# Optimization experiments

Hardware: AMD Instinct MI355X
Metric: run time of the kernel (lower is better)

The kernel has to match this reference:

```python
import jax, jax.numpy as jnp
import numpy as np

N = 1000000          # total nodes (events)
F = 64               # node feature dim
E = 4000000          # total edges
NB = 16              # number of graphs in batch
GRID = 64            # voxels per spatial dim; voxel_size = 1/GRID over [0,1)^2
VOXEL_SIZE = 1.0 / GRID
S = NB * GRID * GRID # fixed cluster-id space (batch-major voxel ids)


def setup_inputs() -> dict:
    key = jax.random.key(0)
    k1, k2, k3, k4 = jax.random.split(key, 4)
    x = jax.random.normal(k1, (N, F), dtype=jnp.float32)
    pos = jax.random.uniform(k2, (N, 2), dtype=jnp.float32)
    batch = jnp.sort(jax.random.randint(k3, (N,), 0, NB, dtype=jnp.int32))
    edge_index = jax.random.randint(k4, (2, E), 0, N, dtype=jnp.int32)
    return {"x": x, "pos": pos, "batch": batch, "edge_index": edge_index}


def reference(x, pos, batch, edge_index):
    # ---- voxel_grid: hash each node into a (batch, vy, vx) voxel cluster ----
    start = pos.min(axis=0)                                   # PyG uses global min as grid origin
    vox = jnp.clip(jnp.floor((pos - start) / VOXEL_SIZE).astype(jnp.int32), 0, GRID - 1)
    cluster = batch * (GRID * GRID) + vox[:, 1] * GRID + vox[:, 0]   # [N]

    # ---- max_pool: scatter-max features, scatter-mean positions ----
    x_pool = jax.ops.segment_max(x, cluster, num_segments=S)         # [S, F]
    count = jax.ops.segment_sum(jnp.ones((x.shape[0],), x.dtype), cluster, num_segments=S)
    node_valid = count > 0                                           # empty voxels masked
    x_pool = jnp.where(node_valid[:, None], x_pool, 0.0)
    pos_pool = jax.ops.segment_sum(pos, cluster, num_segments=S) / jnp.maximum(count, 1.0)[:, None]

    # ---- edge coarsening: map to clusters, drop self-loops, coalesce dups ----
    c_row = cluster[edge_index[0]]
    c_col = cluster[edge_index[1]]
    order = jnp.lexsort((c_col, c_row))                              # sort pairs (row primary)
    r = c_row[order]
    c = c_col[order]
    first = jnp.concatenate([jnp.array([True]), (r[1:] != r[:-1]) | (c[1:] != c[:-1])])
    edge_valid = first & (r != c)                                    # dedup + remove self-loops
    e_row = jnp.where(edge_valid, r, 0)
    e_col = jnp.where(edge_valid, c, 0)

    # ---- transform = Cartesian(norm=True, cat=False) on pooled positions ----
    cart = pos_pool[e_row] - pos_pool[e_col]                         # [E, 2]
    cart = jnp.where(edge_valid[:, None], cart, 0.0)
    max_val = jnp.max(jnp.abs(cart))
    edge_attr = jnp.where(edge_valid[:, None], cart / (2.0 * max_val) + 0.5, 0.0)

    return x_pool, pos_pool, jnp.stack([e_row, e_col]), edge_attr, edge_valid
```

## Files before the change

### kernel.cpp

```cpp
#include <hip/hip_runtime.h>
#include <math.h>

static constexpr int F     = 64;
static constexpr int GRIDV = 64;
static constexpr int SEG   = 16 * GRIDV * GRIDV;
static constexpr int MINB  = 256;
static constexpr int GPART = 512;
static constexpr int PTHR  = 512;
static constexpr int NBIN  = 512;
static constexpr int BSH   = 23;
static constexpr int ETBL  = NBIN * GPART;
static constexpr int SCAP  = 10240;
static constexpr int NGP   = 512;
static constexpr int NTH   = 256;
static constexpr int NTBL  = NBIN * NGP;

typedef float __attribute__((ext_vector_type(4))) f32x4;

__device__ __forceinline__ float wave_min(float v) {
    for (int o = 32; o > 0; o >>= 1) v = fminf(v, __shfl_down(v, o));
    return v;
}
__device__ __forceinline__ float wave_max(float v) {
    for (int o = 32; o > 0; o >>= 1) v = fmaxf(v, __shfl_down(v, o));
    return v;
}
__device__ __forceinline__ f32x4 vmax4(f32x4 a, f32x4 b) {
    f32x4 r;
    r.x = fmaxf(a.x, b.x); r.y = fmaxf(a.y, b.y);
    r.z = fmaxf(a.z, b.z); r.w = fmaxf(a.w, b.w);
    return r;
}

template <int NT>
__device__ __forceinline__ unsigned block_incl_scan(unsigned v, int t) {
    __shared__ unsigned wsum[NT / 64];
    int lane = t & 63, w = t >> 6;
    unsigned sc = v;
    #pragma unroll
    for (int o = 1; o < 64; o <<= 1) {
        unsigned u = __shfl_up(sc, o);
        if (lane >= o) sc += u;
    }
    if (lane == 63) wsum[w] = sc;
    __syncthreads();
    if (w == 0 && lane < NT / 64) {
        unsigned ws = wsum[lane];
        #pragma unroll
        for (int o = 1; o < NT / 64; o <<= 1) {
            unsigned u = __shfl_up(ws, o);
            if (lane >= o) ws += u;
        }
        wsum[lane] = ws;
    }
    __syncthreads();
    return sc + ((w > 0) ? wsum[w - 1] : 0u);
}

__global__ void k_min(const float2* __restrict__ pos, int n, float2* __restrict__ pmin) {
    __shared__ float shx[4], shy[4];
    int stride = gridDim.x * blockDim.x;
    float mx = INFINITY, my = INFINITY;
    for (int i = blockIdx.x * blockDim.x + threadIdx.x; i < n; i += stride) {
        float2 p = pos[i];
        mx = fminf(mx, p.x); my = fminf(my, p.y);
    }
    mx = wave_min(mx); my = wave_min(my);
    int w = threadIdx.x >> 6;
    if ((threadIdx.x & 63) == 0) { shx[w] = mx; shy[w] = my; }
    __syncthreads();
    if (threadIdx.x == 0) {
        mx = fminf(fminf(shx[0], shx[1]), fminf(shx[2], shx[3]));
        my = fminf(fminf(shy[0], shy[1]), fminf(shy[2], shy[3]));
        pmin[blockIdx.x] = make_float2(mx, my);
    }
}

__global__ void k_minred(const float2* __restrict__ pmin, int nb, unsigned* hdr) {
    __shared__ float shx[4], shy[4];
    int t = threadIdx.x;
    float mx = INFINITY, my = INFINITY;
    for (int i = t; i < nb; i += blockDim.x) {
        float2 p = pmin[i];
        mx = fminf(mx, p.x); my = fminf(my, p.y);
    }
    mx = wave_min(mx); my = wave_min(my);
    int w = t >> 6;
    if ((t & 63) == 0) { shx[w] = mx; shy[w] = my; }
    __syncthreads();
    if (t == 0) {
        int nw = (int)(blockDim.x + 63) >> 6;
        for (int i = 1; i < nw; ++i) { mx = fminf(mx, shx[i]); my = fminf(my, shy[i]); }
        hdr[0] = (unsigned)__float_as_int(mx);
        hdr[1] = (unsigned)__float_as_int(my);
    }
}

__global__ __launch_bounds__(NTH) void k_cluster(const float2* __restrict__ pos,
                          const int* __restrict__ batch, int n,
                          const unsigned* __restrict__ hdr, int* __restrict__ cl,
                          unsigned* __restrict__ ntable) {
    __shared__ unsigned hist[NBIN];
    int t = threadIdx.x, b = blockIdx.x;
    for (int j = t; j < NBIN; j += NTH) hist[j] = 0u;
    __syncthreads();
    float sx = __int_as_float((int)hdr[0]);
    float sy = __int_as_float((int)hdr[1]);
    for (int i = b * NTH + t; i < n; i += NGP * NTH) {
        float2 p = pos[i];
        int vx = min(max((int)floorf((p.x - sx) * 64.0f), 0), GRIDV - 1);
        int vy = min(max((int)floorf((p.y - sy) * 64.0f), 0), GRIDV - 1);
        int c = batch[i] * (GRIDV * GRIDV) + vy * GRIDV + vx;
        cl[i] = c;
        atomicAdd(&hist[(unsigned)c >> 7], 1u);
    }
    __syncthreads();
    for (int j = t; j < NBIN; j += NTH) ntable[j * NGP + b] = hist[j];
}

__global__ void k_scan1(const unsigned* __restrict__ cnt, unsigned* __restrict__ off,
                        unsigned* __restrict__ blksum) {
    int t = threadIdx.x;
    int g = blockIdx.x * 1024 + t;
    unsigned v = cnt[g];
    unsigned incl = block_incl_scan<1024>(v, t);
    off[g] = incl - v;
    if (t == 1023) blksum[blockIdx.x] = incl;
}

__global__ void k_scan_add(unsigned* __restrict__ off, const unsigned* __restrict__ blksum,
                           int nblk, int n, unsigned total) {
    __shared__ unsigned sh[256];
    int t = threadIdx.x, b = blockIdx.x;
    if (t < 256) sh[t] = (t < b && t < nblk) ? blksum[t] : 0u;
    __syncthreads();
    for (int s = 128; s > 0; s >>= 1) {
        if (t < s) sh[t] += sh[t + s];
        __syncthreads();
    }
    off[b * 1024 + t] += sh[0];
    if (b == 0 && t == 0) off[n] = total;
}

__global__ __launch_bounds__(NTH) void k_npart(const int* __restrict__ cl,
                       const float2* __restrict__ pos, int n,
                       const unsigned* __restrict__ ntable,
                       unsigned* __restrict__ pc, unsigned* __restrict__ pn,
                       float2* __restrict__ ppos) {
    __shared__ unsigned stage_c[2048], stage_n[2048];
    __shared__ float stage_px[2048], stage_py[2048];
    __shared__ unsigned h[NBIN], cur[NBIN], tbl_s[NBIN];
    int t = threadIdx.x, b = blockIdx.x;
    for (int j = t; j < NBIN; j += NTH) {
        unsigned a = ntable[j * NGP + b];
        tbl_s[j] = a;
        h[j] = ntable[j * NGP + b + 1] - a;
    }
    __syncthreads();
    unsigned a0 = h[2 * t], a1 = h[2 * t + 1];
    unsigned incl = block_incl_scan<NTH>(a0 + a1, t);
    unsigned base = incl - (a0 + a1);
    cur[2 * t] = base;
    cur[2 * t + 1] = base + a0;
    __syncthreads();
    for (int i = b * NTH + t; i < n; i += NGP * NTH) {
        unsigned c = (unsigned)cl[i];
        float2 p = pos[i];
        unsigned q = atomicAdd(&cur[c >> 7], 1u);
        stage_c[q] = c; stage_n[q] = (unsigned)i;
        stage_px[q] = p.x; stage_py[q] = p.y;
    }
    __syncthreads();
    int cnt = (int)cur[NBIN - 1];
    for (int j = t; j < cnt; j += NTH) {
        unsigned c = stage_c[j];
        unsigned bin = c >> 7;
        unsigned start = cur[bin] - h[bin];
        unsigned g = tbl_s[bin] + ((unsigned)j - start);
        pc[g] = c; pn[g] = stage_n[j];
        ppos[g] = make_float2(stage_px[j], stage_py[j]);
    }
}

__global__ __launch_bounds__(256) void k_ngroup(const unsigned* __restrict__ pc,
                         const unsigned* __restrict__ pn, const float2* __restrict__ ppos,
                         const unsigned* __restrict__ ntable, int n,
                         unsigned* __restrict__ node_off, int* __restrict__ node_sorted,
                         float2* __restrict__ out_pos) {
    __shared__ unsigned cnt[128], sc[128], cur[128];
    __shared__ float psx[128], psy[128];
    int b = blockIdx.x, t = threadIdx.x;
    if (t < 128) { cnt[t] = 0u; psx[t] = 0.f; psy[t] = 0.f; }
    __syncthreads();
    int beg = (int)ntable[b * NGP];
    int end = (int)ntable[(b + 1) * NGP];
    for (int i = beg + t; i < end; i += 256) {
        unsigned c = pc[i] & 127u;
        float2 p = ppos[i];
        atomicAdd(&cnt[c], 1u);
        atomicAdd(&psx[c], p.x);
        atomicAdd(&psy[c], p.y);
    }
    __syncthreads();
    if (t < 128) sc[t] = cnt[t];
    __syncthreads();
    for (int s = 1; s < 128; s <<= 1) {
        unsigned u = (t >= s && t < 128) ? sc[t - s] : 0u;
        __syncthreads();
        if (t < 128) sc[t] += u;
        __syncthreads();
    }
    if (t < 128) {
        unsigned basec = (unsigned)beg + sc[t] - cnt[t];
        node_off[b * 128 + t] = basec;
        cur[t] = basec;
        unsigned c2 = cnt[t];
        out_pos[b * 128 + t] = c2 ? make_float2(psx[t] / (float)c2, psy[t] / (float)c2)
                                  : make_float2(0.f, 0.f);
    }
    if (b == NBIN - 1 && t == 0) node_off[SEG] = (unsigned)n;
    __syncthreads();
    for (int i = beg + t; i < end; i += 256) {
        unsigned c = pc[i] & 127u;
        unsigned slot = atomicAdd(&cur[c], 1u);
        node_sorted[slot] = (int)pn[i];
    }
}

__global__ __launch_bounds__(256) void k_pool(const float* __restrict__ x,
                      const int* __restrict__ node_sorted, const unsigned* __restrict__ off,
                      float* __restrict__ out_x) {
    int wid  = threadIdx.x >> 6;
    int lane = threadIdx.x & 63;
    int s = blockIdx.x * 4 + wid;
    unsigned beg = off[s], end = off[s + 1];
    int g   = lane >> 4;
    int cl4 = (lane & 15) << 2;
    f32x4 m0, m1, m2, m3;
    m0.x = m0.y = m0.z = m0.w = -INFINITY;
    m1 = m0; m2 = m0; m3 = m0;
    for (unsigned base = beg; base < end; base += 64) {
        int m = (int)min(64u, end - base);
        int nd_my = (lane < m) ? node_sorted[base + lane] : 0;
        int last = m - 1;
        int K = (m + 15) >> 4;
        for (int k = 0; k < K; ++k) {
            int j = g + (k << 4);
            int j0 = min(j, last);
            int j1 = min(j + 4, last);
            int j2 = min(j + 8, last);
            int j3 = min(j + 12, last);
            int n0 = __shfl(nd_my, j0);
            int n1 = __shfl(nd_my, j1);
            int n2 = __shfl(nd_my, j2);
            int n3 = __shfl(nd_my, j3);
            f32x4 v0 = __builtin_nontemporal_load((const f32x4*)&x[(size_t)n0 * F + cl4]);
            f32x4 v1 = __builtin_nontemporal_load((const f32x4*)&x[(size_t)n1 * F + cl4]);
            f32x4 v2 = __builtin_nontemporal_load((const f32x4*)&x[(size_t)n2 * F + cl4]);
            f32x4 v3 = __builtin_nontemporal_load((const f32x4*)&x[(size_t)n3 * F + cl4]);
            m0 = vmax4(m0, v0);
            m1 = vmax4(m1, v1);
            m2 = vmax4(m2, v2);
            m3 = vmax4(m3, v3);
        }
    }
    m0 = vmax4(vmax4(m0, m1), vmax4(m2, m3));
    #pragma unroll
    for (int o = 16; o <= 32; o <<= 1) {
        m0.x = fmaxf(m0.x, __shfl_xor(m0.x, o));
        m0.y = fmaxf(m0.y, __shfl_xor(m0.y, o));
        m0.z = fmaxf(m0.z, __shfl_xor(m0.z, o));
        m0.w = fmaxf(m0.w, __shfl_xor(m0.w, o));
    }
    if (g == 0) {
        f32x4 r;
        if (end > beg) r = m0;
        else { r.x = r.y = r.z = r.w = 0.f; }
        *(f32x4*)&out_x[(size_t)s * F + cl4] = r;
    }
}

__global__ __launch_bounds__(PTHR) void k_ehist(const int* __restrict__ ei, int e,
                        const int* __restrict__ cl,
                        unsigned* __restrict__ keysA, unsigned* __restrict__ etable) {
    __shared__ unsigned hist[NBIN];
    int t = threadIdx.x, b = blockIdx.x;
    for (int j = t; j < NBIN; j += PTHR) hist[j] = 0u;
    __syncthreads();
    for (int i = b * PTHR + t; i < e; i += GPART * PTHR) {
        unsigned r = (unsigned)cl[ei[i]];
        unsigned c = (unsigned)cl[ei[e + i]];
        unsigned k = (r << 16) | c;
        keysA[i] = k;
        atomicAdd(&hist[k >> BSH], 1u);
    }
    __syncthreads();
    for (int j = t; j < NBIN; j += PTHR) etable[j * GPART + b] = hist[j];
}

__global__ __launch_bounds__(PTHR) void k_partition(const unsigned* __restrict__ keysA, int e,
                            const unsigned* __restrict__ etable,
                            unsigned* __restrict__ keysB) {
    __shared__ unsigned stage[8192];
    __shared__ unsigned h[NBIN], cur[NBIN], tbl_s[NBIN];
    int t = threadIdx.x, b = blockIdx.x;
    unsigned a = etable[t * GPART + b];
    unsigned hv = etable[t * GPART + b + 1] - a;
    tbl_s[t] = a;
    h[t] = hv;
    __syncthreads();
    unsigned incl = block_incl_scan<PTHR>(hv, t);
    cur[t] = incl - hv;
    __syncthreads();
    for (int i = b * PTHR + t; i < e; i += GPART * PTHR) {
        unsigned k = keysA[i];
        unsigned p = atomicAdd(&cur[k >> BSH], 1u);
        stage[p] = k;
    }
    __syncthreads();
    int cnt = (int)cur[NBIN - 1];
    for (int j = t; j < cnt; j += PTHR) {
        unsigned k = stage[j];
        unsigned bin = k >> BSH;
        unsigned start = cur[bin] - h[bin];
        keysB[tbl_s[bin] + ((unsigned)j - start)] = k;
    }
}

__global__ __launch_bounds__(512) void k_subsort(const unsigned* __restrict__ src,
                         unsigned* __restrict__ scratch, const unsigned* __restrict__ table,
                         const float2* __restrict__ pos_pool,
                         float* __restrict__ out_erow, float* __restrict__ out_ecol,
                         float* __restrict__ out_valid, float2* __restrict__ out_attr,
                         float* __restrict__ pmax) {
    __shared__ unsigned hist[8192];
    __shared__ unsigned stage[SCAP];
    __shared__ float shm[8];
    int b = blockIdx.x, t = threadIdx.x;
    int beg = (int)table[b * GPART];
    int end = (int)table[(b + 1) * GPART];
    int len = end - beg;
    if (len <= 0) { if (t == 0) pmax[b] = 0.f; return; }
    for (int j = t; j < 8192; j += 512) hist[j] = 0u;
    __syncthreads();
    for (int i = beg + t; i < end; i += 512) {
        unsigned d = (src[i] >> 10) & 8191u;
        atomicAdd(&hist[((d & 15u) << 9) | (d >> 4)], 1u);
    }
    __syncthreads();
    unsigned loc[16];
    unsigned s = 0;
    #pragma unroll
    for (int u = 0; u < 16; ++u) { loc[u] = s; s += hist[u * 512 + t]; }
    unsigned incl = block_incl_scan<512>(s, t);
    bool inlds = (len <= SCAP);
    unsigned base0 = (inlds ? 0u : (unsigned)beg) + incl - s;
    #pragma unroll
    for (int u = 0; u < 16; ++u) hist[u * 512 + t] = base0 + loc[u];
    __syncthreads();
    float am = 0.f;
    if (inlds) {
        for (int i = beg + t; i < end; i += 512) {
            unsigned k = src[i];
            unsigned d = (k >> 10) & 8191u;
            stage[atomicAdd(&hist[((d & 15u) << 9) | (d >> 4)], 1u)] = k;
        }
        __syncthreads();
        for (int j = t; j < len; j += 512) {
            unsigned hi = stage[j] >> 10;
            if (j > 0 && (stage[j - 1] >> 10) == hi) continue;
            int rend = j + 1;
            while (rend < len && (stage[rend] >> 10) == hi) ++rend;
            for (int a2 = j + 1; a2 < rend; ++a2) {
                unsigned v = stage[a2]; int c = a2 - 1;
                while (c >= j && stage[c] > v) { stage[c + 1] = stage[c]; --c; }
                stage[c + 1] = v;
            }
        }
        __syncthreads();
        for (int j = t; j < len; j += 512) {
            unsigned k = stage[j];
            bool first = (j == 0) || (stage[j - 1] != k);
            unsigned r = k >> 16, c = k & 0xFFFFu;
            bool valid = first && (r != c);
            float ax, ay;
            if (valid) {
                float2 pr = pos_pool[r], pcc = pos_pool[c];
                ax = pr.x - pcc.x; ay = pr.y - pcc.y;
                am = fmaxf(am, fmaxf(fabsf(ax), fabsf(ay)));
            } else {
                ax = __int_as_float(0x7FC00000); ay = 0.f;
            }
            out_erow[beg + j]  = valid ? (float)r : 0.f;
            out_ecol[beg + j]  = valid ? (float)c : 0.f;
            out_valid[beg + j] = valid ? 1.f : 0.f;
            out_attr[beg + j]  = make_float2(ax, ay);
        }
    } else {
        for (int i = beg + t; i < end; i += 512) {
            unsigned k = src[i];
            unsigned d = (k >> 10) & 8191u;
            scratch[atomicAdd(&hist[((d & 15u) << 9) | (d >> 4)], 1u)] = k;
        }
        __threadfence();
        __syncthreads();
        for (int j = beg + t; j < end; j += 512) {
            unsigned hi = scratch[j] >> 10;
            if (j > beg && (scratch[j - 1] >> 10) == hi) continue;
            int rend = j + 1;
            while (rend < end && (scratch[rend] >> 10) == hi) ++rend;
            for (int a2 = j + 1; a2 < rend; ++a2) {
                unsigned v = scratch[a2]; int c = a2 - 1;
                while (c >= j && scratch[c] > v) { scratch[c + 1] = scratch[c]; --c; }
                scratch[c + 1] = v;
            }
        }
        __threadfence();
        __syncthreads();
        for (int j = beg + t; j < end; j += 512) {
            unsigned k = scratch[j];
            bool first = (j == beg) || (scratch[j - 1] != k);
            unsigned r = k >> 16, c = k & 0xFFFFu;
            bool valid = first && (r != c);
            float ax, ay;
            if (valid) {
                float2 pr = pos_pool[r], pcc = pos_pool[c];
                ax = pr.x - pcc.x; ay = pr.y - pcc.y;
                am = fmaxf(am, fmaxf(fabsf(ax), fabsf(ay)));
            } else {
                ax = __int_as_float(0x7FC00000); ay = 0.f;
            }
            out_erow[j]  = valid ? (float)r : 0.f;
            out_ecol[j]  = valid ? (float)c : 0.f;
            out_valid[j] = valid ? 1.f : 0.f;
            out_attr[j]  = make_float2(ax, ay);
        }
    }
    am = wave_max(am);
    if ((t & 63) == 0) shm[t >> 6] = am;
    __syncthreads();
    if (t == 0) {
        float m = shm[0];
        #pragma unroll
        for (int i2 = 1; i2 < 8; ++i2) m = fmaxf(m, shm[i2]);
        pmax[b] = m;
    }
}

__global__ __launch_bounds__(256) void k_rescale(float2* __restrict__ out_attr, int e,
                                                 const float* __restrict__ pmax) {
    __shared__ float shm[4];
    int t = threadIdx.x;
    float m = fmaxf(pmax[t], pmax[t + 256]);
    m = wave_max(m);
    if ((t & 63) == 0) shm[t >> 6] = m;
    __syncthreads();
    float denom = 2.0f * fmaxf(fmaxf(shm[0], shm[1]), fmaxf(shm[2], shm[3]));
    int i = blockIdx.x * blockDim.x + t;
    if (i >= e) return;
    float2 a = out_attr[i];
    bool valid = (a.x == a.x);
    float ax = valid ? a.x / denom + 0.5f : 0.f;
    float ay = valid ? a.y / denom + 0.5f : 0.f;
    out_attr[i] = make_float2(ax, ay);
}

extern "C" void kernel_launch(void* const* d_in, const int* in_sizes, int n_in,
                              void* d_out, int out_size, void* d_ws, size_t ws_size,
                              hipStream_t stream) {
    const float* x    = (const float*)d_in[0];
    const float* pos  = (const float*)d_in[1];
    const int* batch  = (const int*)d_in[2];
    const int* ei     = (const int*)d_in[3];
    const int n = in_sizes[2];
    const int e = in_sizes[3] / 2;

    float* out      = (float*)d_out;
    float* out_x    = out;
    float* out_pos  = out_x  + (size_t)SEG * F;
    float* out_erow = out_pos + (size_t)SEG * 2;
    float* out_ecol = out_erow + e;
    float* out_attr = out_ecol + e;
    float* out_val  = out_attr + (size_t)2 * e;

    const int nb_e = (e + 255) / 256;

    char* w = (char*)d_ws;
    unsigned* hdr         = (unsigned*)w;
    int*      cl          = (int*)(w + 256);
    int*      node_sorted = (int*)(w + 256 + (size_t)n * 4);
    unsigned* node_off    = (unsigned*)(w + 256 + (size_t)n * 8);
    unsigned* table       = node_off + SEG + 1;
    unsigned* keysA       = table + ETBL + 1;
    unsigned* keysB       = keysA + e;
    float2*   ppos        = (float2*)(keysB + e);
    unsigned* blksum      = (unsigned*)(ppos + n);
    float2*   pmin        = (float2*)(blksum + 256);
    float*    pmax        = (float*)(pmin + MINB);
    unsigned* ntable      = table;
    unsigned* pc          = keysA;
    unsigned* pn          = keysB;

    k_min<<<MINB, 256, 0, stream>>>((const float2*)pos, n, pmin);
    k_minred<<<1, 256, 0, stream>>>(pmin, MINB, hdr);
    k_cluster<<<NGP, NTH, 0, stream>>>((const float2*)pos, batch, n, hdr, cl, ntable);
    k_scan1<<<NTBL / 1024, 1024, 0, stream>>>(ntable, ntable, blksum);
    k_scan_add<<<NTBL / 1024, 1024, 0, stream>>>(ntable, blksum, NTBL / 1024, NTBL, (unsigned)n);
    k_npart<<<NGP, NTH, 0, stream>>>(cl, (const float2*)pos, n, ntable, pc, pn, ppos);
    k_ngroup<<<NBIN, 256, 0, stream>>>(pc, pn, ppos, ntable, n, node_off, node_sorted,
                                       (float2*)out_pos);
    k_pool<<<SEG / 4, 256, 0, stream>>>(x, node_sorted, node_off, out_x);
    k_ehist<<<GPART, PTHR, 0, stream>>>(ei, e, cl, keysA, table);
    k_scan1<<<ETBL / 1024, 1024, 0, stream>>>(table, table, blksum);
    k_scan_add<<<ETBL / 1024, 1024, 0, stream>>>(table, blksum, ETBL / 1024, ETBL, (unsigned)e);
    k_partition<<<GPART, PTHR, 0, stream>>>(keysA, e, table, keysB);
    k_subsort<<<NBIN, 512, 0, stream>>>(keysB, keysA, table, (const float2*)out_pos,
                                        out_erow, out_ecol, out_val, (float2*)out_attr, pmax);
    k_rescale<<<nb_e, 256, 0, stream>>>((float2*)out_attr, e, pmax);
}
```

Baseline: 239.7 us.

## Merge node and edge histogram scans, atomic min, and split edge output pass

Replaces the two-stage min reduction with a global atomicMin, removing one launch. The node and edge bucket tables are concatenated so a single scan pass serves both, with a bias subtracted on the edge side. The subsort kernel now writes only the sorted keys and the abs-max of the Cartesian offsets. A new output kernel recomputes validity and the normalized attributes from the sorted keys, which removes the intermediate NaN-marked attribute write and its re-read. The cost is an extra key read, duplicate pos_pool gathers, and a larger scan.

```diff
diff --git a/kernel.cpp b/kernel.cpp
--- a/kernel.cpp
+++ b/kernel.cpp
@@ -14,6 +14,7 @@
 static constexpr int NGP   = 512;
 static constexpr int NTH   = 256;
 static constexpr int NTBL  = NBIN * NGP;
+static constexpr int JTBL  = NTBL + ETBL;
 
 typedef float __attribute__((ext_vector_type(4))) f32x4;
 
@@ -57,7 +58,12 @@
     return sc + ((w > 0) ? wsum[w - 1] : 0u);
 }
 
-__global__ void k_min(const float2* __restrict__ pos, int n, float2* __restrict__ pmin) {
+__global__ void k_hdrinit(unsigned* hdr) {
+    hdr[0] = 0x7F800000u;
+    hdr[1] = 0x7F800000u;
+}
+
+__global__ void k_min(const float2* __restrict__ pos, int n, unsigned* hdr) {
     __shared__ float shx[4], shy[4];
     int stride = gridDim.x * blockDim.x;
     float mx = INFINITY, my = INFINITY;
@@ -72,27 +78,8 @@
     if (threadIdx.x == 0) {
         mx = fminf(fminf(shx[0], shx[1]), fminf(shx[2], shx[3]));
         my = fminf(fminf(shy[0], shy[1]), fminf(shy[2], shy[3]));
-        pmin[blockIdx.x] = make_float2(mx, my);
-    }
-}
-
-__global__ void k_minred(const float2* __restrict__ pmin, int nb, unsigned* hdr) {
-    __shared__ float shx[4], shy[4];
-    int t = threadIdx.x;
-    float mx = INFINITY, my = INFINITY;
-    for (int i = t; i < nb; i += blockDim.x) {
-        float2 p = pmin[i];
-        mx = fminf(mx, p.x); my = fminf(my, p.y);
-    }
-    mx = wave_min(mx); my = wave_min(my);
-    int w = t >> 6;
-    if ((t & 63) == 0) { shx[w] = mx; shy[w] = my; }
-    __syncthreads();
-    if (t == 0) {
-        int nw = (int)(blockDim.x + 63) >> 6;
-        for (int i = 1; i < nw; ++i) { mx = fminf(mx, shx[i]); my = fminf(my, shy[i]); }
-        hdr[0] = (unsigned)__float_as_int(mx);
-        hdr[1] = (unsigned)__float_as_int(my);
+        atomicMin((int*)&hdr[0], __float_as_int(mx));
+        atomicMin((int*)&hdr[1], __float_as_int(my));
     }
 }
 
@@ -118,6 +105,24 @@
     for (int j = t; j < NBIN; j += NTH) ntable[j * NGP + b] = hist[j];
 }
 
+__global__ __launch_bounds__(PTHR) void k_ehist(const int* __restrict__ ei, int e,
+                        const int* __restrict__ cl,
+                        unsigned* __restrict__ keysA, unsigned* __restrict__ etbl) {
+    __shared__ unsigned hist[NBIN];
+    int t = threadIdx.x, b = blockIdx.x;
+    for (int j = t; j < NBIN; j += PTHR) hist[j] = 0u;
+    __syncthreads();
+    for (int i = b * PTHR + t; i < e; i += GPART * PTHR) {
+        unsigned r = (unsigned)cl[ei[i]];
+        unsigned c = (unsigned)cl[ei[e + i]];
+        unsigned k = (r << 16) | c;
+        keysA[i] = k;
+        atomicAdd(&hist[k >> BSH], 1u);
+    }
+    __syncthreads();
+    for (int j = t; j < NBIN; j += PTHR) etbl[j * GPART + b] = hist[j];
+}
+
 __global__ void k_scan1(const unsigned* __restrict__ cnt, unsigned* __restrict__ off,
                         unsigned* __restrict__ blksum) {
     int t = threadIdx.x;
@@ -129,17 +134,17 @@
 }
 
 __global__ void k_scan_add(unsigned* __restrict__ off, const unsigned* __restrict__ blksum,
-                           int nblk, int n, unsigned total) {
-    __shared__ unsigned sh[256];
+                           int nblk, int nent, unsigned total) {
+    __shared__ unsigned sh[512];
     int t = threadIdx.x, b = blockIdx.x;
-    if (t < 256) sh[t] = (t < b && t < nblk) ? blksum[t] : 0u;
-    __syncthreads();
-    for (int s = 128; s > 0; s >>= 1) {
+    if (t < 512) sh[t] = (t < b && t < nblk) ? blksum[t] : 0u;
+    __syncthreads();
+    for (int s = 256; s > 0; s >>= 1) {
         if (t < s) sh[t] += sh[t + s];
         __syncthreads();
     }
     off[b * 1024 + t] += sh[0];
-    if (b == 0 && t == 0) off[n] = total;
+    if (b == 0 && t == 0) off[nent] = total;
 }
 
 __global__ __launch_bounds__(NTH) void k_npart(const int* __restrict__ cl,
@@ -280,32 +285,14 @@
     }
 }
 
-__global__ __launch_bounds__(PTHR) void k_ehist(const int* __restrict__ ei, int e,
-                        const int* __restrict__ cl,
-                        unsigned* __restrict__ keysA, unsigned* __restrict__ etable) {
-    __shared__ unsigned hist[NBIN];
-    int t = threadIdx.x, b = blockIdx.x;
-    for (int j = t; j < NBIN; j += PTHR) hist[j] = 0u;
-    __syncthreads();
-    for (int i = b * PTHR + t; i < e; i += GPART * PTHR) {
-        unsigned r = (unsigned)cl[ei[i]];
-        unsigned c = (unsigned)cl[ei[e + i]];
-        unsigned k = (r << 16) | c;
-        keysA[i] = k;
-        atomicAdd(&hist[k >> BSH], 1u);
-    }
-    __syncthreads();
-    for (int j = t; j < NBIN; j += PTHR) etable[j * GPART + b] = hist[j];
-}
-
 __global__ __launch_bounds__(PTHR) void k_partition(const unsigned* __restrict__ keysA, int e,
-                            const unsigned* __restrict__ etable,
+                            const unsigned* __restrict__ etbl, unsigned bias,
                             unsigned* __restrict__ keysB) {
     __shared__ unsigned stage[8192];
     __shared__ unsigned h[NBIN], cur[NBIN], tbl_s[NBIN];
     int t = threadIdx.x, b = blockIdx.x;
-    unsigned a = etable[t * GPART + b];
-    unsigned hv = etable[t * GPART + b + 1] - a;
+    unsigned a = etbl[t * GPART + b] - bias;
+    unsigned hv = (etbl[t * GPART + b + 1] - bias) - a;
     tbl_s[t] = a;
     h[t] = hv;
     __syncthreads();
@@ -328,17 +315,15 @@
 }
 
 __global__ __launch_bounds__(512) void k_subsort(const unsigned* __restrict__ src,
-                         unsigned* __restrict__ scratch, const unsigned* __restrict__ table,
-                         const float2* __restrict__ pos_pool,
-                         float* __restrict__ out_erow, float* __restrict__ out_ecol,
-                         float* __restrict__ out_valid, float2* __restrict__ out_attr,
+                         unsigned* __restrict__ dst, const unsigned* __restrict__ etbl,
+                         unsigned bias, const float2* __restrict__ pos_pool,
                          float* __restrict__ pmax) {
     __shared__ unsigned hist[8192];
     __shared__ unsigned stage[SCAP];
     __shared__ float shm[8];
     int b = blockIdx.x, t = threadIdx.x;
-    int beg = (int)table[b * GPART];
-    int end = (int)table[(b + 1) * GPART];
+    int beg = (int)(etbl[b * GPART] - bias);
+    int end = (int)(etbl[(b + 1) * GPART] - bias);
     int len = end - beg;
     if (len <= 0) { if (t == 0) pmax[b] = 0.f; return; }
     for (int j = t; j < 8192; j += 512) hist[j] = 0u;
@@ -380,60 +365,43 @@
         __syncthreads();
         for (int j = t; j < len; j += 512) {
             unsigned k = stage[j];
+            dst[beg + j] = k;
             bool first = (j == 0) || (stage[j - 1] != k);
             unsigned r = k >> 16, c = k & 0xFFFFu;
-            bool valid = first && (r != c);
-            float ax, ay;
-            if (valid) {
+            if (first && r != c) {
                 float2 pr = pos_pool[r], pcc = pos_pool[c];
-                ax = pr.x - pcc.x; ay = pr.y - pcc.y;
-                am = fmaxf(am, fmaxf(fabsf(ax), fabsf(ay)));
-            } else {
-                ax = __int_as_float(0x7FC00000); ay = 0.f;
+                am = fmaxf(am, fmaxf(fabsf(pr.x - pcc.x), fabsf(pr.y - pcc.y)));
             }
-            out_erow[beg + j]  = valid ? (float)r : 0.f;
-            out_ecol[beg + j]  = valid ? (float)c : 0.f;
-            out_valid[beg + j] = valid ? 1.f : 0.f;
-            out_attr[beg + j]  = make_float2(ax, ay);
         }
     } else {
         for (int i = beg + t; i < end; i += 512) {
             unsigned k = src[i];
             unsigned d = (k >> 10) & 8191u;
-            scratch[atomicAdd(&hist[((d & 15u) << 9) | (d >> 4)], 1u)] = k;
+            dst[atomicAdd(&hist[((d & 15u) << 9) | (d >> 4)], 1u)] = k;
         }
         __threadfence();
         __syncthreads();
         for (int j = beg + t; j < end; j += 512) {
-            unsigned hi = scratch[j] >> 10;
-            if (j > beg && (scratch[j - 1] >> 10) == hi) continue;
+            unsigned hi = dst[j] >> 10;
+            if (j > beg && (dst[j - 1] >> 10) == hi) continue;
             int rend = j + 1;
-            while (rend < end && (scratch[rend] >> 10) == hi) ++rend;
+            while (rend < end && (dst[rend] >> 10) == hi) ++rend;
             for (int a2 = j + 1; a2 < rend; ++a2) {
-                unsigned v = scratch[a2]; int c = a2 - 1;
-                while (c >= j && scratch[c] > v) { scratch[c + 1] = scratch[c]; --c; }
-                scratch[c + 1] = v;
+                unsigned v = dst[a2]; int c = a2 - 1;
+                while (c >= j && dst[c] > v) { dst[c + 1] = dst[c]; --c; }
+                dst[c + 1] = v;
             }
         }
         __threadfence();
         __syncthreads();
         for (int j = beg + t; j < end; j += 512) {
-            unsigned k = scratch[j];
-            bool first = (j == beg) || (scratch[j - 1] != k);
+            unsigned k = dst[j];
+            bool first = (j == beg) || (dst[j - 1] != k);
             unsigned r = k >> 16, c = k & 0xFFFFu;
-            bool valid = first && (r != c);
-            float ax, ay;
-            if (valid) {
+            if (first && r != c) {
                 float2 pr = pos_pool[r], pcc = pos_pool[c];
-                ax = pr.x - pcc.x; ay = pr.y - pcc.y;
-                am = fmaxf(am, fmaxf(fabsf(ax), fabsf(ay)));
-            } else {
-                ax = __int_as_float(0x7FC00000); ay = 0.f;
+                am = fmaxf(am, fmaxf(fabsf(pr.x - pcc.x), fabsf(pr.y - pcc.y)));
             }
-            out_erow[j]  = valid ? (float)r : 0.f;
-            out_ecol[j]  = valid ? (float)c : 0.f;
-            out_valid[j] = valid ? 1.f : 0.f;
-            out_attr[j]  = make_float2(ax, ay);
         }
     }
     am = wave_max(am);
@@ -447,8 +415,10 @@
     }
 }
 
-__global__ __launch_bounds__(256) void k_rescale(float2* __restrict__ out_attr, int e,
-                                                 const float* __restrict__ pmax) {
+__global__ __launch_bounds__(256) void k_eout(const unsigned* __restrict__ keys, int e,
+                         const float2* __restrict__ pos_pool, const float* __restrict__ pmax,
+                         float* __restrict__ out_erow, float* __restrict__ out_ecol,
+                         float* __restrict__ out_valid, float2* __restrict__ out_attr) {
     __shared__ float shm[4];
     int t = threadIdx.x;
     float m = fmaxf(pmax[t], pmax[t + 256]);
@@ -458,11 +428,20 @@
     float denom = 2.0f * fmaxf(fmaxf(shm[0], shm[1]), fmaxf(shm[2], shm[3]));
     int i = blockIdx.x * blockDim.x + t;
     if (i >= e) return;
-    float2 a = out_attr[i];
-    bool valid = (a.x == a.x);
-    float ax = valid ? a.x / denom + 0.5f : 0.f;
-    float ay = valid ? a.y / denom + 0.5f : 0.f;
-    out_attr[i] = make_float2(ax, ay);
+    unsigned k = keys[i];
+    bool first = (i == 0) || (keys[i - 1] != k);
+    unsigned r = k >> 16, c = k & 0xFFFFu;
+    bool valid = first && (r != c);
+    float ax = 0.f, ay = 0.f;
+    if (valid) {
+        float2 pr = pos_pool[r], pcc = pos_pool[c];
+        ax = (pr.x - pcc.x) / denom + 0.5f;
+        ay = (pr.y - pcc.y) / denom + 0.5f;
+    }
+    out_erow[i]  = valid ? (float)r : 0.f;
+    out_ecol[i]  = valid ? (float)c : 0.f;
+    out_valid[i] = valid ? 1.f : 0.f;
+    out_attr[i]  = make_float2(ax, ay);
 }
 
 extern "C" void kernel_launch(void* const* d_in, const int* in_sizes, int n_in,
@@ -491,30 +470,30 @@
     int*      node_sorted = (int*)(w + 256 + (size_t)n * 4);
     unsigned* node_off    = (unsigned*)(w + 256 + (size_t)n * 8);
     unsigned* table       = node_off + SEG + 1;
-    unsigned* keysA       = table + ETBL + 1;
+    unsigned* keysA       = table + JTBL + 1;
     unsigned* keysB       = keysA + e;
-    float2*   ppos        = (float2*)(keysB + e);
+    unsigned* pc          = keysB + e;
+    unsigned* pn          = pc + n;
+    float2*   ppos        = (float2*)(pn + n);
     unsigned* blksum      = (unsigned*)(ppos + n);
-    float2*   pmin        = (float2*)(blksum + 256);
-    float*    pmax        = (float*)(pmin + MINB);
+    float*    pmax        = (float*)(blksum + 512);
     unsigned* ntable      = table;
-    unsigned* pc          = keysA;
-    unsigned* pn          = keysB;
-
-    k_min<<<MINB, 256, 0, stream>>>((const float2*)pos, n, pmin);
-    k_minred<<<1, 256, 0, stream>>>(pmin, MINB, hdr);
+    unsigned* etbl        = table + NTBL;
+
+    k_hdrinit<<<1, 1, 0, stream>>>(hdr);
+    k_min<<<MINB, 256, 0, stream>>>((const float2*)pos, n, hdr);
     k_cluster<<<NGP, NTH, 0, stream>>>((const float2*)pos, batch, n, hdr, cl, ntable);
-    k_scan1<<<NTBL / 1024, 1024, 0, stream>>>(ntable, ntable, blksum);
-    k_scan_add<<<NTBL / 1024, 1024, 0, stream>>>(ntable, blksum, NTBL / 1024, NTBL, (unsigned)n);
+    k_ehist<<<GPART, PTHR, 0, stream>>>(ei, e, cl, keysA, etbl);
+    k_scan1<<<JTBL / 1024, 1024, 0, stream>>>(table, table, blksum);
+    k_scan_add<<<JTBL / 1024, 1024, 0, stream>>>(table, blksum, JTBL / 1024, JTBL,
+                                                 (unsigned)(n + e));
     k_npart<<<NGP, NTH, 0, stream>>>(cl, (const float2*)pos, n, ntable, pc, pn, ppos);
     k_ngroup<<<NBIN, 256, 0, stream>>>(pc, pn, ppos, ntable, n, node_off, node_sorted,
                                        (float2*)out_pos);
+    k_partition<<<GPART, PTHR, 0, stream>>>(keysA, e, etbl, (unsigned)n, keysB);
+    k_subsort<<<NBIN, 512, 0, stream>>>(keysB, keysA, etbl, (unsigned)n,
+                                        (const float2*)out_pos, pmax);
     k_pool<<<SEG / 4, 256, 0, stream>>>(x, node_sorted, node_off, out_x);
-    k_ehist<<<GPART, PTHR, 0, stream>>>(ei, e, cl, keysA, table);
-    k_scan1<<<ETBL / 1024, 1024, 0, stream>>>(table, table, blksum);
-    k_scan_add<<<ETBL / 1024, 1024, 0, stream>>>(table, blksum, ETBL / 1024, ETBL, (unsigned)e);
-    k_partition<<<GPART, PTHR, 0, stream>>>(keysA, e, table, keysB);
-    k_subsort<<<NBIN, 512, 0, stream>>>(keysB, keysA, table, (const float2*)out_pos,
-                                        out_erow, out_ecol, out_val, (float2*)out_attr, pmax);
-    k_rescale<<<nb_e, 256, 0, stream>>>((float2*)out_attr, e, pmax);
-}
+    k_eout<<<nb_e, 256, 0, stream>>>(keysA, e, (const float2*)out_pos, pmax,
+                                     out_erow, out_ecol, out_val, (float2*)out_attr);
+}
```

New measurement: 248.9 us. +3.8%, slower.
